# Kernel tuning notes

Measured on AMD Instinct MI355X. Metric: run time of the kernel, lower is better.

Reference implementation:

```python
import jax, jax.numpy as jnp
import numpy as np

CH = 512
NH = 8
EPS = 1e-5

def setup_inputs() -> dict:
    key = jax.random.key(0)
    ks = jax.random.split(key, 7)
    x = jax.random.normal(ks[0], (1, CH, 64, 64), dtype=jnp.float32)
    norm_w = jnp.ones((CH,), jnp.float32)
    norm_b = jnp.zeros((CH,), jnp.float32)
    s1 = 1.0 / np.sqrt(CH)
    qkv_w = jax.random.uniform(ks[1], (3 * CH, CH), jnp.float32, -s1, s1)
    qkv_b = jax.random.uniform(ks[2], (3 * CH,), jnp.float32, -s1, s1)
    proj_w = jax.random.uniform(ks[3], (CH, CH), jnp.float32, -s1, s1)
    proj_b = jax.random.uniform(ks[4], (CH,), jnp.float32, -s1, s1)
    return {"x": x, "norm_w": norm_w, "norm_b": norm_b, "qkv_w": qkv_w,
            "qkv_b": qkv_b, "proj_w": proj_w, "proj_b": proj_b}

def _forward(x, norm_w, norm_b, qkv_w, qkv_b, proj_w, proj_b):
    B, C, H, W = x.shape
    G = 32
    # GroupNorm(32, C) + SiLU
    xg = x.reshape(B, G, C // G, H, W)
    mu = jnp.mean(xg, axis=(2, 3, 4), keepdims=True)
    var = jnp.var(xg, axis=(2, 3, 4), keepdims=True)
    h = ((xg - mu) * jax.lax.rsqrt(var + EPS)).reshape(B, C, H, W)
    h = h * norm_w[None, :, None, None] + norm_b[None, :, None, None]
    h = jax.nn.silu(h)
    N = H * W
    h = h.reshape(B, C, N)
    # qkv 1x1 conv == channel matmul
    qkv = jnp.einsum('oc,bcn->bon', qkv_w, h) + qkv_b[None, :, None]
    q, k, v = jnp.split(qkv, 3, axis=1)  # each (B, C, N)
    d = C // NH
    # faithful to torch: transpose(1,2) then row-major reshape
    q = q.transpose(0, 2, 1).reshape(B * NH, N, d)
    k = k.transpose(0, 2, 1).reshape(B * NH, N, d)
    v = v.transpose(0, 2, 1).reshape(B * NH, N, d)
    scale = d ** (-0.5)
    attn = jax.nn.softmax(jnp.einsum('bnd,bmd->bnm', q, k) * scale, axis=-1)
    out = jnp.einsum('bnm,bmd->bnd', attn, v)
    out = out.reshape(B, N, C).transpose(0, 2, 1)  # (B, C, N)
    out = jnp.einsum('oc,bcn->bon', proj_w, out) + proj_b[None, :, None]
    return x + out.reshape(B, C, H, W)

def reference(x, norm_w, norm_b, qkv_w, qkv_b, proj_w, proj_b):
    return _forward(x, norm_w, norm_b, qkv_w, qkv_b, proj_w, proj_b)
```

## Files before the change

kernel.cpp:

```cpp
#include <hip/hip_runtime.h>

typedef __attribute__((ext_vector_type(8)))  short s16x8;
typedef __attribute__((ext_vector_type(4)))  float f32x4;
typedef __attribute__((ext_vector_type(16))) float f32x16;
typedef __attribute__((ext_vector_type(4)))  unsigned int u32x4;

#define CHN 512
#define NSP 4096

__device__ __forceinline__ ushort f2b(float f){
  unsigned u = __builtin_bit_cast(unsigned, f);
  u = (u + 0x7fffu + ((u >> 16) & 1u)) >> 16;
  return (ushort)u;
}
__device__ __forceinline__ float b2f(ushort u){
  return __builtin_bit_cast(float, ((unsigned)u) << 16);
}

__device__ __forceinline__ s16x8 ldfrag(const void* p){
  return *reinterpret_cast<const s16x8*>(p);
}

__device__ __forceinline__ f32x4 mfma16(s16x8 a, s16x8 b, f32x4 c){
  return __builtin_amdgcn_mfma_f32_16x16x32_bf16(a, b, c, 0, 0, 0);
}
__device__ __forceinline__ f32x16 mfma32(s16x8 a, s16x8 b, f32x16 c){
  return __builtin_amdgcn_mfma_f32_32x32x16_bf16(a, b, c, 0, 0, 0);
}
__device__ __forceinline__ unsigned cvtpk(float lo, float hi){
  unsigned r;
  asm("v_cvt_pk_bf16_f32 %0, %1, %2" : "=v"(r) : "v"(lo), "v"(hi));
  return r;
}
__device__ __forceinline__ void gload16(const void* g, void* l){
  __builtin_amdgcn_global_load_lds(
      (const __attribute__((address_space(1))) unsigned int*)g,
      (__attribute__((address_space(3))) unsigned int*)l, 16, 0, 0);
}
__device__ __forceinline__ ushort4 f4b(float4 v){
  ushort4 o;
  o.x = f2b(v.x); o.y = f2b(v.y); o.z = f2b(v.z); o.w = f2b(v.w);
  return o;
}

__global__ __launch_bounds__(256) void prep(const float4* __restrict__ qkvw, const float4* __restrict__ projw,
                                            const float* __restrict__ x,
                                            ushort4* __restrict__ Wq, ushort4* __restrict__ Wp,
                                            float* __restrict__ part){
  int b = blockIdx.x;
  if (b < 768){
    int i = b*256 + threadIdx.x;
    Wq[i] = f4b(qkvw[i]);
  } else if (b < 1024){
    int i = (b-768)*256 + threadIdx.x;
    Wp[i] = f4b(projw[i]);
  } else {
    int pb = b - 1024;
    const float4* p = reinterpret_cast<const float4*>(x + (size_t)pb * 8192);
    float s = 0.f, s2 = 0.f;
    #pragma unroll
    for (int i = 0; i < 8; ++i){
      float4 v = p[threadIdx.x + i*256];
      s  += v.x + v.y + v.z + v.w;
      s2 += v.x*v.x + v.y*v.y + v.z*v.z + v.w*v.w;
    }
    #pragma unroll
    for (int off = 32; off > 0; off >>= 1){ s += __shfl_down(s, off); s2 += __shfl_down(s2, off); }
    __shared__ float ls[4], ls2[4];
    int wv = threadIdx.x >> 6;
    if ((threadIdx.x & 63) == 0){ ls[wv] = s; ls2[wv] = s2; }
    __syncthreads();
    if (threadIdx.x == 0){
      part[pb*2]     = ls[0]+ls[1]+ls[2]+ls[3];
      part[pb*2 + 1] = ls2[0]+ls2[1]+ls2[2]+ls2[3];
    }
  }
}

__global__ __launch_bounds__(256) void norm_apply(const float* __restrict__ x, const float* __restrict__ part,
                                                  const float* __restrict__ nw, const float* __restrict__ nb,
                                                  ushort* __restrict__ h_t){
  __shared__ float tile[64][65];
  __shared__ float smu[32], srs[32];
  if (threadIdx.x < 32){
    int g = threadIdx.x;
    float s = 0.f, s2 = 0.f;
    #pragma unroll
    for (int i = 0; i < 8; ++i){ s += part[(g*8+i)*2]; s2 += part[(g*8+i)*2+1]; }
    float mu  = s * (1.f/65536.f);
    float var = s2 * (1.f/65536.f) - mu*mu;
    smu[g] = mu;
    srs[g] = rsqrtf(var + 1e-5f);
  }
  __syncthreads();
  int ct0 = (blockIdx.x >> 6) << 6;
  int nt0 = (blockIdx.x & 63) << 6;
  int tc = threadIdx.x >> 6;
  int tn = threadIdx.x & 63;
  #pragma unroll
  for (int rr = 0; rr < 16; ++rr){
    int cl = rr*4 + tc;
    int c  = ct0 + cl;
    float v  = x[(size_t)c * NSP + nt0 + tn];
    float hn = (v - smu[c >> 4]) * srs[c >> 4] * nw[c] + nb[c];
    float sv = hn / (1.f + __expf(-hn));
    tile[tn][cl] = sv;
  }
  __syncthreads();
  #pragma unroll
  for (int rr = 0; rr < 16; ++rr){
    int nl = rr*4 + tc;
    h_t[(size_t)(nt0 + nl) * CHN + ct0 + tn] = f2b(tile[nl][tn]);
  }
}

template<int MODE, int BM, int BN>
__global__ __launch_bounds__(256) void gemm_tn(
    const ushort* __restrict__ A, const ushort* __restrict__ Bw,
    const float* __restrict__ bias, const float* __restrict__ xres,
    ushort* __restrict__ qS, ushort* __restrict__ kF, ushort* __restrict__ vF,
    float* __restrict__ outF)
{
  constexpr int RW = BM/2, CW = BN/2;
  constexpr int MI = RW/16, NJ = CW/16;
  __shared__ __align__(16) ushort As[2][BM*32];
  __shared__ __align__(16) ushort Bs[2][BN*32];
  int tid = threadIdx.x;
  int lane = tid & 63, wv = tid >> 6;
  int lr = lane & 15, lg = lane >> 4;
  int wr = wv >> 1, wc = wv & 1;
  int nbB = blockIdx.x * BM;
  int obB = blockIdx.y * BN;
  int nb = nbB + wr*RW, ob = obB + wc*CW;
  f32x4 acc[MI][NJ] = {};

  const ushort* Ag = A  + (size_t)(nbB + (tid>>2))*CHN + (tid&3)*8;
  const ushort* Bg = Bw + (size_t)(obB + (tid>>2))*CHN + (tid&3)*8;

  #define GSTAGE(BUF, KK) {                                                    \
    _Pragma("unroll") for (int ii = 0; ii < BM/64; ++ii)                       \
      gload16(Ag + (size_t)ii*64*CHN + (KK), &As[BUF][ii*2048 + tid*8]);       \
    _Pragma("unroll") for (int ii = 0; ii < BN/64; ++ii)                       \
      gload16(Bg + (size_t)ii*64*CHN + (KK), &Bs[BUF][ii*2048 + tid*8]); }

  GSTAGE(0, 0);
  asm volatile("s_waitcnt vmcnt(0)" ::: "memory");
  __syncthreads();
  int cur = 0;
  for (int kk = 0; kk < CHN; kk += 32){
    if (kk < CHN-32) GSTAGE(cur^1, kk+32);
    s16x8 af[MI], bf[NJ];
    #pragma unroll
    for (int t = 0; t < MI; ++t) af[t] = *(const s16x8*)&As[cur][(wr*RW + lr + t*16)*32 + lg*8];
    #pragma unroll
    for (int t = 0; t < NJ; ++t) bf[t] = *(const s16x8*)&Bs[cur][(wc*CW + lr + t*16)*32 + lg*8];
    #pragma unroll
    for (int i = 0; i < MI; ++i)
      #pragma unroll
      for (int j = 0; j < NJ; ++j)
        acc[i][j] = mfma16(af[i], bf[j], acc[i][j]);
    asm volatile("s_waitcnt vmcnt(0)" ::: "memory");
    __syncthreads();
    cur ^= 1;
  }
  #undef GSTAGE

  if (MODE == 0){
    #pragma unroll
    for (int j = 0; j < NJ; ++j){
      int o = ob + j*16 + lr;
      float bs = bias[o];
      int sec = o >> 9;
      int co  = o & 511;
      int bb = co >> 6, dd = co & 63;
      if (sec == 0){
        const float qsc = 0.18033688011112042f;
        #pragma unroll
        for (int i = 0; i < MI; ++i){
          int n0 = nb + i*16 + lg*4;
          int hh = n0 >> 9, aa = n0 & 511;
          size_t base = ((size_t)((hh<<3)+bb)*512 + aa)*64 + dd;
          #pragma unroll
          for (int r = 0; r < 4; ++r)
            qS[base + (size_t)r*64] = f2b((acc[i][j][r] + bs) * qsc);
        }
      } else if (sec == 1){
        int s = dd >> 4, khi = (dd >> 3) & 1, off = dd & 7;
        #pragma unroll
        for (int i = 0; i < MI; ++i){
          int n0 = nb + i*16 + lg*4;
          int hh = n0 >> 9, aa = n0 & 511;
          int T = bb*16 + (aa >> 5);
          size_t widx = ((((size_t)hh*128 + T)*4 + s)*64 + (aa & 31) + 32*khi)*8 + off;
          #pragma unroll
          for (int r = 0; r < 4; ++r)
            kF[widx + (size_t)r*8] = f2b(acc[i][j][r] + bs);
        }
      } else {
        int l31v = dd & 31, fh = dd >> 5;
        #pragma unroll
        for (int i = 0; i < MI; ++i){
          int n0 = nb + i*16 + lg*4;
          int hh = n0 >> 9, aa = n0 & 511;
          int T = bb*16 + (aa >> 5);
          int w = aa & 31;
          int f = fh*2 + (w >> 4);
          int vhi = (w >> 3) & 1, koff = w & 7;
          size_t widx = ((((size_t)hh*128 + T)*4 + f)*64 + l31v + 32*vhi)*8 + koff;
          ushort4 pk;
          pk.x = f2b(acc[i][j][0] + bs);
          pk.y = f2b(acc[i][j][1] + bs);
          pk.z = f2b(acc[i][j][2] + bs);
          pk.w = f2b(acc[i][j][3] + bs);
          *reinterpret_cast<ushort4*>(vF + widx) = pk;
        }
      }
    }
  } else {
    #pragma unroll
    for (int j = 0; j < NJ; ++j){
      int o = ob + j*16 + lr;
      float bs = bias[o];
      #pragma unroll
      for (int i = 0; i < MI; ++i){
        int n0 = nb + i*16 + lg*4;
        f32x4 xr = *reinterpret_cast<const f32x4*>(xres + (size_t)o*NSP + n0);
        f32x4 ov;
        #pragma unroll
        for (int r = 0; r < 4; ++r) ov[r] = acc[i][j][r] + bs + xr[r];
        *reinterpret_cast<f32x4*>(outF + (size_t)o*NSP + n0) = ov;
      }
    }
  }
}

__global__ __launch_bounds__(512) void flash9(
    const ushort* __restrict__ qS, const ushort* __restrict__ kF,
    const ushort* __restrict__ vF, ushort* __restrict__ attnT)
{
  __shared__ __align__(16) ushort ldsK[4][2][2048];
  __shared__ __align__(16) float llds[3][64];
  __shared__ __align__(16) float winv[64];
  int lane = threadIdx.x & 63, wv = threadIdx.x >> 6;
  int l31 = lane & 31, hi = lane >> 5;
  int qg = wv & 1, kvh = wv >> 1;
  int bx = (blockIdx.x & 7) * 64 + (blockIdx.x >> 3);
  int hh    = bx >> 6;
  int b1    = (bx >> 3) & 7;
  int chunk = bx & 7;
  int a0 = chunk * 64 + qg * 32;

  const ushort* qp = qS + ((size_t)((hh*8 + b1)*512) + a0 + l31)*64 + hi*8;
  s16x8 qf0 = ldfrag(qp), qf1 = ldfrag(qp+16), qf2 = ldfrag(qp+32), qf3 = ldfrag(qp+48);

  f32x16 O0 = {}, O1 = {};
  f32x4 lacc = {};
  s16x8 v0, v1, v2, v3;

  size_t tbase = (size_t)hh*262144 + (size_t)(kvh*32)*2048;

  #define STAGEK(BUF, T) {                                                     \
    const ushort* ks_ = kF + tbase + (size_t)(T)*2048 + qg*1024 + lane*8;      \
    ushort* lk_ = &ldsK[kvh][BUF][qg*1024 + lane*8];                           \
    gload16(ks_,       lk_);                                                   \
    gload16(ks_ + 512, lk_ + 512); }

  #define LOADV(T) {                                                           \
    const ushort* vp_ = vF + tbase + (size_t)(T)*2048 + lane*8;                \
    v0 = ldfrag(vp_);        v1 = ldfrag(vp_ + 512);                           \
    v2 = ldfrag(vp_ + 1024); v3 = ldfrag(vp_ + 1536); }

  #define COMPUTE(BUF) {                                                       \
    const ushort* kc = &ldsK[kvh][BUF][lane*8];                                \
    s16x8 k0 = *(const s16x8*)(kc),        k1 = *(const s16x8*)(kc +  512);    \
    s16x8 k2 = *(const s16x8*)(kc + 1024), k3 = *(const s16x8*)(kc + 1536);    \
    f32x16 S = {};                                                             \
    S = mfma32(k0, qf0, S); S = mfma32(k1, qf1, S);                            \
    S = mfma32(k2, qf2, S); S = mfma32(k3, qf3, S);                            \
    float p[16];                                                               \
    _Pragma("unroll") for (int r = 0; r < 16; ++r)                             \
      p[r] = __builtin_amdgcn_exp2f(S[r]);                                     \
    lacc[0] += (p[0]+p[1])   + (p[2]+p[3]);                                    \
    lacc[1] += (p[4]+p[5])   + (p[6]+p[7]);                                    \
    lacc[2] += (p[8]+p[9])   + (p[10]+p[11]);                                  \
    lacc[3] += (p[12]+p[13]) + (p[14]+p[15]);                                  \
    unsigned A0 = cvtpk(p[0],p[1]),  A1 = cvtpk(p[2],p[3]);                    \
    unsigned B0 = cvtpk(p[4],p[5]),  B1 = cvtpk(p[6],p[7]);                    \
    asm("v_permlane32_swap_b32 %0, %1" : "+v"(A0), "+v"(B0));                  \
    asm("v_permlane32_swap_b32 %0, %1" : "+v"(A1), "+v"(B1));                  \
    unsigned C0 = cvtpk(p[8],p[9]),  C1 = cvtpk(p[10],p[11]);                  \
    unsigned D0 = cvtpk(p[12],p[13]),D1 = cvtpk(p[14],p[15]);                  \
    asm("v_permlane32_swap_b32 %0, %1" : "+v"(C0), "+v"(D0));                  \
    asm("v_permlane32_swap_b32 %0, %1" : "+v"(C1), "+v"(D1));                  \
    u32x4 w1 = {A0, A1, B0, B1}, w2 = {C0, C1, D0, D1};                        \
    s16x8 pa1 = __builtin_bit_cast(s16x8, w1);                                 \
    s16x8 pa2 = __builtin_bit_cast(s16x8, w2);                                 \
    O0 = mfma32(pa1, v0, O0); O0 = mfma32(pa2, v1, O0);                        \
    O1 = mfma32(pa1, v2, O1); O1 = mfma32(pa2, v3, O1);                        \
  }

  STAGEK(0, 0);
  __builtin_amdgcn_sched_barrier(0);
  LOADV(0);
  asm volatile("s_waitcnt vmcnt(4)" ::: "memory");
  __syncthreads();
  int cur = 0;
  for (int t = 0; t < 32; ++t){
    if (t < 31){
      STAGEK(cur^1, t+1);
      __builtin_amdgcn_sched_barrier(0);
    }
    COMPUTE(cur);
    if (t < 31){
      LOADV(t+1);
      asm volatile("s_waitcnt vmcnt(4)" ::: "memory");
    }
    __syncthreads();
    cur ^= 1;
  }
  #undef STAGEK
  #undef LOADV
  #undef COMPUTE

  float ts = (lacc[0]+lacc[1]) + (lacc[2]+lacc[3]);
  float tu = ts, tv = ts;
  asm("v_permlane32_swap_b32 %0, %1" : "+v"(tu), "+v"(tv));
  float lrun = tu + tv;

  if (kvh < 3){
    ushort* park = &ldsK[kvh][0][0];
    #pragma unroll
    for (int g = 0; g < 4; ++g)
      #pragma unroll
      for (int r4 = 0; r4 < 4; ++r4){
        int fr = qg*32 + g*8 + hi*4 + r4;
        park[fr*64 + l31]      = f2b(O0[g*4+r4]);
        park[fr*64 + l31 + 32] = f2b(O1[g*4+r4]);
      }
    if (hi == 0) llds[kvh][qg*32 + l31] = lrun;
  }
  __syncthreads();
  if (kvh == 3){
    if (hi == 0){
      int idx = qg*32 + l31;
      winv[idx] = 1.0f / (llds[0][idx] + llds[1][idx] + llds[2][idx] + lrun);
    }
    asm volatile("s_waitcnt lgkmcnt(0)" ::: "memory");
    const ushort* p0 = &ldsK[0][0][0];
    const ushort* p1 = &ldsK[1][0][0];
    const ushort* p2 = &ldsK[2][0][0];
    size_t colBase = (size_t)b1*64 + l31;
    #pragma unroll
    for (int g = 0; g < 4; ++g){
      f32x4 iv = *reinterpret_cast<const f32x4*>(&winv[qg*32 + g*8 + hi*4]);
      #pragma unroll
      for (int r4 = 0; r4 < 4; ++r4){
        int row = g*8 + hi*4 + r4;
        int fr = qg*32 + row;
        float o0 = (b2f(p0[fr*64 + l31]) + b2f(p1[fr*64 + l31])
                  + b2f(p2[fr*64 + l31]) + O0[g*4+r4]) * iv[r4];
        float o1 = (b2f(p0[fr*64 + l31 + 32]) + b2f(p1[fr*64 + l31 + 32])
                  + b2f(p2[fr*64 + l31 + 32]) + O1[g*4+r4]) * iv[r4];
        size_t base = ((size_t)(hh*512 + a0 + row))*CHN + colBase;
        attnT[base]      = f2b(o0);
        attnT[base + 32] = f2b(o1);
      }
    }
  }
}

extern "C" void kernel_launch(void* const* d_in, const int* in_sizes, int n_in,
                              void* d_out, int out_size, void* d_ws, size_t ws_size,
                              hipStream_t stream)
{
  (void)in_sizes; (void)n_in; (void)out_size; (void)ws_size;
  const float* x     = (const float*)d_in[0];
  const float* normw = (const float*)d_in[1];
  const float* normb = (const float*)d_in[2];
  const float* qkvw  = (const float*)d_in[3];
  const float* qkvb  = (const float*)d_in[4];
  const float* projw = (const float*)d_in[5];
  const float* projb = (const float*)d_in[6];
  float* out = (float*)d_out;

  char* w = (char*)d_ws;
  ushort* h_t  = (ushort*)(w + 1024);
  ushort* Wq   = (ushort*)(w + 1024 + 4194304);
  ushort* Wp   = (ushort*)(w + 1024 + 4194304 + 1572864);
  ushort* qSb  = (ushort*)(w + 1024 + 4194304 + 1572864 + 524288);
  ushort* kFb  = qSb + 2097152;
  ushort* vFb  = kFb + 2097152;
  float*  part = (float*)(vFb + 2097152);
  ushort* attnT = h_t;

  prep<<<1280, 256, 0, stream>>>((const float4*)qkvw, (const float4*)projw, x,
                                 (ushort4*)Wq, (ushort4*)Wp, part);
  norm_apply<<<512, 256, 0, stream>>>(x, part, normw, normb, h_t);
  gemm_tn<0,128,128><<<dim3(32, 12), 256, 0, stream>>>(h_t, Wq, qkvb, nullptr, qSb, kFb, vFb, nullptr);
  flash9<<<512, 512, 0, stream>>>(qSb, kFb, vFb, attnT);
  gemm_tn<1,64,64><<<dim3(64, 8), 256, 0, stream>>>(attnT, Wp, projb, x, nullptr, nullptr, nullptr, out);
}
```

Measured before the change: 85.25 us.

## Split attention KV range across two blocks and combine partials in new kernel

The flash attention kernel now splits each query chunk's key range into two halves handled by separate blocks, doubling the grid from 512 to 1024 blocks. Each block writes unnormalized bf16 partial outputs and row sums, and a new combine kernel adds the two halves and normalizes. The QKV GEMM tile width is also halved to double its grid. This aims at better CU occupancy on the many-CU GPU, at the cost of an extra launch, extra global traffic for partials, and an added bf16 rounding of the partial sums.

```diff
diff --git a/kernel.cpp b/kernel.cpp
--- a/kernel.cpp
+++ b/kernel.cpp
@@ -234,20 +234,22 @@
   }
 }
 
-__global__ __launch_bounds__(512) void flash9(
+__global__ __launch_bounds__(512) void flash10(
     const ushort* __restrict__ qS, const ushort* __restrict__ kF,
-    const ushort* __restrict__ vF, ushort* __restrict__ attnT)
+    const ushort* __restrict__ vF, ushort* __restrict__ pO0,
+    ushort* __restrict__ pO1, float* __restrict__ lsum)
 {
   __shared__ __align__(16) ushort ldsK[4][2][2048];
   __shared__ __align__(16) float llds[3][64];
-  __shared__ __align__(16) float winv[64];
   int lane = threadIdx.x & 63, wv = threadIdx.x >> 6;
   int l31 = lane & 31, hi = lane >> 5;
   int qg = wv & 1, kvh = wv >> 1;
-  int bx = (blockIdx.x & 7) * 64 + (blockIdx.x >> 3);
-  int hh    = bx >> 6;
-  int b1    = (bx >> 3) & 7;
-  int chunk = bx & 7;
+  int bx = (blockIdx.x & 7) * 128 + (blockIdx.x >> 3);
+  int hh    = bx >> 7;
+  int rem   = bx & 127;
+  int b1    = rem >> 4;
+  int chunk = (rem >> 1) & 7;
+  int half  = rem & 1;
   int a0 = chunk * 64 + qg * 32;
 
   const ushort* qp = qS + ((size_t)((hh*8 + b1)*512) + a0 + l31)*64 + hi*8;
@@ -257,7 +259,7 @@
   f32x4 lacc = {};
   s16x8 v0, v1, v2, v3;
 
-  size_t tbase = (size_t)hh*262144 + (size_t)(kvh*32)*2048;
+  size_t tbase = (size_t)hh*262144 + (size_t)(half*64 + kvh*16)*2048;
 
   #define STAGEK(BUF, T) {                                                     \
     const ushort* ks_ = kF + tbase + (size_t)(T)*2048 + qg*1024 + lane*8;      \
@@ -305,13 +307,13 @@
   asm volatile("s_waitcnt vmcnt(4)" ::: "memory");
   __syncthreads();
   int cur = 0;
-  for (int t = 0; t < 32; ++t){
-    if (t < 31){
+  for (int t = 0; t < 16; ++t){
+    if (t < 15){
       STAGEK(cur^1, t+1);
       __builtin_amdgcn_sched_barrier(0);
     }
     COMPUTE(cur);
-    if (t < 31){
+    if (t < 15){
       LOADV(t+1);
       asm volatile("s_waitcnt vmcnt(4)" ::: "memory");
     }
@@ -341,32 +343,56 @@
   }
   __syncthreads();
   if (kvh == 3){
-    if (hi == 0){
-      int idx = qg*32 + l31;
-      winv[idx] = 1.0f / (llds[0][idx] + llds[1][idx] + llds[2][idx] + lrun);
-    }
-    asm volatile("s_waitcnt lgkmcnt(0)" ::: "memory");
     const ushort* p0 = &ldsK[0][0][0];
     const ushort* p1 = &ldsK[1][0][0];
     const ushort* p2 = &ldsK[2][0][0];
+    ushort* pO = half ? pO1 : pO0;
     size_t colBase = (size_t)b1*64 + l31;
     #pragma unroll
     for (int g = 0; g < 4; ++g){
-      f32x4 iv = *reinterpret_cast<const f32x4*>(&winv[qg*32 + g*8 + hi*4]);
       #pragma unroll
       for (int r4 = 0; r4 < 4; ++r4){
         int row = g*8 + hi*4 + r4;
         int fr = qg*32 + row;
-        float o0 = (b2f(p0[fr*64 + l31]) + b2f(p1[fr*64 + l31])
-                  + b2f(p2[fr*64 + l31]) + O0[g*4+r4]) * iv[r4];
-        float o1 = (b2f(p0[fr*64 + l31 + 32]) + b2f(p1[fr*64 + l31 + 32])
-                  + b2f(p2[fr*64 + l31 + 32]) + O1[g*4+r4]) * iv[r4];
+        float o0 = b2f(p0[fr*64 + l31]) + b2f(p1[fr*64 + l31])
+                 + b2f(p2[fr*64 + l31]) + O0[g*4+r4];
+        float o1 = b2f(p0[fr*64 + l31 + 32]) + b2f(p1[fr*64 + l31 + 32])
+                 + b2f(p2[fr*64 + l31 + 32]) + O1[g*4+r4];
         size_t base = ((size_t)(hh*512 + a0 + row))*CHN + colBase;
-        attnT[base]      = f2b(o0);
-        attnT[base + 32] = f2b(o1);
+        pO[base]      = f2b(o0);
+        pO[base + 32] = f2b(o1);
       }
     }
-  }
+    if (b1 == 0 && hi == 0){
+      int idx = qg*32 + l31;
+      lsum[half*4096 + hh*512 + chunk*64 + idx] =
+          llds[0][idx] + llds[1][idx] + llds[2][idx] + lrun;
+    }
+  }
+}
+
+__global__ __launch_bounds__(256) void att_combine(const ushort* pO0, const ushort* pO1,
+                                                   const float* __restrict__ lsum, ushort* attnT){
+  int g = blockIdx.x * 256 + threadIdx.x;
+  int n = g >> 6;
+  int c = (g & 63) * 8;
+  size_t idx = (size_t)n * CHN + c;
+  float inv = 1.0f / (lsum[n] + lsum[4096 + n]);
+  ushort4 a0 = *reinterpret_cast<const ushort4*>(pO0 + idx);
+  ushort4 a1 = *reinterpret_cast<const ushort4*>(pO0 + idx + 4);
+  ushort4 b0 = *reinterpret_cast<const ushort4*>(pO1 + idx);
+  ushort4 b1 = *reinterpret_cast<const ushort4*>(pO1 + idx + 4);
+  ushort4 o0, o1;
+  o0.x = f2b((b2f(a0.x) + b2f(b0.x)) * inv);
+  o0.y = f2b((b2f(a0.y) + b2f(b0.y)) * inv);
+  o0.z = f2b((b2f(a0.z) + b2f(b0.z)) * inv);
+  o0.w = f2b((b2f(a0.w) + b2f(b0.w)) * inv);
+  o1.x = f2b((b2f(a1.x) + b2f(b1.x)) * inv);
+  o1.y = f2b((b2f(a1.y) + b2f(b1.y)) * inv);
+  o1.z = f2b((b2f(a1.z) + b2f(b1.z)) * inv);
+  o1.w = f2b((b2f(a1.w) + b2f(b1.w)) * inv);
+  *reinterpret_cast<ushort4*>(attnT + idx)     = o0;
+  *reinterpret_cast<ushort4*>(attnT + idx + 4) = o1;
 }
 
 extern "C" void kernel_launch(void* const* d_in, const int* in_sizes, int n_in,
@@ -391,12 +417,16 @@
   ushort* kFb  = qSb + 2097152;
   ushort* vFb  = kFb + 2097152;
   float*  part = (float*)(vFb + 2097152);
+  float*  lsum = part + 512;
+  ushort* pO1  = (ushort*)(lsum + 8192);
+  ushort* pO0  = h_t;
   ushort* attnT = h_t;
 
   prep<<<1280, 256, 0, stream>>>((const float4*)qkvw, (const float4*)projw, x,
                                  (ushort4*)Wq, (ushort4*)Wp, part);
   norm_apply<<<512, 256, 0, stream>>>(x, part, normw, normb, h_t);
-  gemm_tn<0,128,128><<<dim3(32, 12), 256, 0, stream>>>(h_t, Wq, qkvb, nullptr, qSb, kFb, vFb, nullptr);
-  flash9<<<512, 512, 0, stream>>>(qSb, kFb, vFb, attnT);
+  gemm_tn<0,128,64><<<dim3(32, 24), 256, 0, stream>>>(h_t, Wq, qkvb, nullptr, qSb, kFb, vFb, nullptr);
+  flash10<<<1024, 512, 0, stream>>>(qSb, kFb, vFb, pO0, pO1, lsum);
+  att_combine<<<1024, 256, 0, stream>>>(pO0, pO1, lsum, attnT);
   gemm_tn<1,64,64><<<dim3(64, 8), 256, 0, stream>>>(attnT, Wp, projb, x, nullptr, nullptr, nullptr, out);
 }
```

Result: slower. 91.00 us (+6.7%).
